# Kernel optimization log

Hardware: AMD Instinct MI355X
Metric: run time of the kernel (lower is better)

## Reference

```python
import jax, jax.numpy as jnp
import numpy as np
import math

B, S, D, H, HD, P = 2, 2048, 2048, 16, 128, 10
ROPE_BASE = 10000.0


def _rope_tables(seq_len, head_dim):
    inv_freq = 1.0 / (ROPE_BASE ** (np.arange(0, head_dim, 2, dtype=np.float32) / head_dim))
    t = np.arange(seq_len, dtype=np.float32)
    freqs = np.outer(t, inv_freq)                  # [S, hd/2]
    emb = np.concatenate([freqs, freqs], axis=-1)  # [S, hd]
    return jnp.asarray(np.cos(emb)), jnp.asarray(np.sin(emb))


def _rotate_half(x):
    half = x.shape[-1] // 2
    return jnp.concatenate([-x[..., half:], x[..., :half]], axis=-1)


def setup_inputs() -> dict:
    key = jax.random.key(0)
    ks = jax.random.split(key, 8)
    hidden_states = jax.random.normal(ks[0], (B, S, D), dtype=jnp.float32)
    # causal additive mask, llama convention: 0 where allowed, large negative above diagonal
    causal = jnp.triu(jnp.full((S, S), -1e9, dtype=jnp.float32), k=1)
    attention_mask = jnp.broadcast_to(causal[None, None], (B, 1, S, S))
    position_ids = jnp.broadcast_to(jnp.arange(S, dtype=jnp.int64)[None], (B, S))
    scale = 1.0 / math.sqrt(D)
    Wq = jax.random.normal(ks[1], (D, D), dtype=jnp.float32) * scale
    Wk = jax.random.normal(ks[2], (D, D), dtype=jnp.float32) * scale
    Wv = jax.random.normal(ks[3], (D, D), dtype=jnp.float32) * scale
    Wo = jax.random.normal(ks[4], (D, D), dtype=jnp.float32) * scale
    adapter_query = jax.random.normal(ks[5], (P, D), dtype=jnp.float32)
    adapter_gate = jax.random.normal(ks[6], (1, H, 1, 1), dtype=jnp.float32) * 0.1
    return dict(hidden_states=hidden_states, attention_mask=attention_mask,
                position_ids=position_ids, Wq=Wq, Wk=Wk, Wv=Wv, Wo=Wo,
                adapter_query=adapter_query, adapter_gate=adapter_gate)


def reference(hidden_states, attention_mask, position_ids, Wq, Wk, Wv, Wo,
              adapter_query, adapter_gate):
    bsz, q_len, _ = hidden_states.shape
    inv_sqrt_hd = 1.0 / math.sqrt(HD)

    def split_heads(x):  # [B,S,D] -> [B,H,S,hd]
        return x.reshape(bsz, q_len, H, HD).transpose(0, 2, 1, 3)

    q = split_heads(hidden_states @ Wq)
    k = split_heads(hidden_states @ Wk)
    v = split_heads(hidden_states @ Wv)

    # RoPE
    cos_t, sin_t = _rope_tables(q_len, HD)
    cos = cos_t[position_ids][:, None]  # [B,1,S,hd]
    sin = sin_t[position_ids][:, None]
    q = q * cos + _rotate_half(q) * sin
    k = k * cos + _rotate_half(k) * sin

    # main attention
    scores = jnp.einsum('bhqd,bhkd->bhqk', q, k) * inv_sqrt_hd
    scores = scores + attention_mask
    attn = jax.nn.softmax(scores.astype(jnp.float32), axis=-1).astype(q.dtype)
    attn_out = jnp.einsum('bhqk,bhkd->bhqd', attn, v)

    # adapter: soft prompt projected through k/v proj (learn_kv=False), no RoPE
    adapter = jnp.broadcast_to(adapter_query[None], (bsz, P, D))  # [B,P,D]
    a_k = (adapter @ Wk).reshape(bsz, P, H, HD).transpose(0, 2, 1, 3)  # [B,H,P,hd]
    a_v = (adapter @ Wv).reshape(bsz, P, H, HD).transpose(0, 2, 1, 3)
    a_scores = jnp.einsum('bhqd,bhpd->bhqp', q, a_k) * inv_sqrt_hd
    a_w = adapter_gate * jax.nn.softmax(a_scores.astype(jnp.float32), axis=-1).astype(q.dtype)
    a_out = jnp.einsum('bhqp,bhpd->bhqd', a_w, a_v)

    out = attn_out + a_out
    out = out.transpose(0, 2, 1, 3).reshape(bsz, q_len, D)
    return out @ Wo
```

## Files before the change

### kernel.cpp

```cpp
#include <hip/hip_runtime.h>
#include <cstdint>
#include <cstddef>
#include <cmath>

typedef __bf16 bf16x8 __attribute__((ext_vector_type(8)));
typedef float  f32x4  __attribute__((ext_vector_type(4)));

__device__ __forceinline__ unsigned short f2bf(float f) {
  unsigned int u = __float_as_uint(f);
  u += 0x7FFF + ((u >> 16) & 1);
  return (unsigned short)(u >> 16);
}
__device__ __forceinline__ float bf2f(unsigned short u) {
  return __uint_as_float(((unsigned int)u) << 16);
}

#define SEQ 2048
#define DMODEL 2048
#define NH 16
#define HD 128
#define NB 2
#define NP 10
#define MAUG 4106
#define SCALEL2 (0.08838834764831845f * 1.44269504088896340f)

#define GLOAD_LDS16(g, l) \
  __builtin_amdgcn_global_load_lds((__attribute__((address_space(1))) const void*)(g), \
                                   (__attribute__((address_space(3))) void*)(l), 16, 0, 0)

#define FENCE() asm volatile("" ::: "memory")
#define SBAR() do { FENCE(); __builtin_amdgcn_s_barrier(); FENCE(); } while (0)
#define WAITVM(N) asm volatile("s_waitcnt vmcnt(" #N ")" ::: "memory")

__global__ void k_tables(float* __restrict__ cost, float* __restrict__ sint) {
  int idx = blockIdx.x * 256 + threadIdx.x;
  if (idx >= SEQ * 64) return;
  int s = idx >> 6, i = idx & 63;
  float invf = expf(-((float)(2 * i) / 128.0f) * logf(10000.0f));
  float a = (float)s * invf;
  float c = cosf(a), sn = sinf(a);
  cost[s * HD + i] = c;  cost[s * HD + 64 + i] = c;
  sint[s * HD + i] = sn; sint[s * HD + 64 + i] = sn;
}

__global__ __launch_bounds__(256) void k_wt(const float* __restrict__ W0,
                                            const float* __restrict__ W1,
                                            const float* __restrict__ W2,
                                            const float* __restrict__ W3,
                                            unsigned short* __restrict__ out) {
  __shared__ float tile[64][65];
  const float* W = (blockIdx.z == 0) ? W0 : (blockIdx.z == 1) ? W1 : (blockIdx.z == 2) ? W2 : W3;
  unsigned short* o = out + (size_t)blockIdx.z * DMODEL * DMODEL;
  int bx = blockIdx.x * 64, by = blockIdx.y * 64;
  int c = threadIdx.x & 15, r0 = threadIdx.x >> 4;
  #pragma unroll
  for (int jj = 0; jj < 4; jj++) {
    int r = r0 + jj * 16;
    float4 v = *(const float4*)&W[(size_t)(bx + r) * DMODEL + by + c * 4];
    tile[r][c * 4 + 0] = v.x; tile[r][c * 4 + 1] = v.y;
    tile[r][c * 4 + 2] = v.z; tile[r][c * 4 + 3] = v.w;
  }
  __syncthreads();
  #pragma unroll
  for (int jj = 0; jj < 4; jj++) {
    int ro = r0 + jj * 16;
    unsigned short s4[4];
    #pragma unroll
    for (int k = 0; k < 4; k++) s4[k] = f2bf(tile[c * 4 + k][ro]);
    *(uint2*)&o[(size_t)(by + ro) * DMODEL + bx + c * 4] = *(const uint2*)s4;
  }
}

__global__ void k_xaug(const float* __restrict__ X, const float* __restrict__ Aq,
                       unsigned short* __restrict__ xaug) {
  size_t u = ((size_t)blockIdx.x * 256 + threadIdx.x) * 8;
  size_t row = u >> 11;
  int col = (int)(u & 2047);
  const float* src = (row < (size_t)NB * SEQ) ? &X[u]
                                              : &Aq[(row - NB * SEQ) * DMODEL + col];
  float4 a = *(const float4*)src;
  float4 b = *(const float4*)(src + 4);
  unsigned short r[8] = { f2bf(a.x), f2bf(a.y), f2bf(a.z), f2bf(a.w),
                          f2bf(b.x), f2bf(b.y), f2bf(b.z), f2bf(b.w) };
  *(uint4*)&xaug[u] = *(const uint4*)r;
}

#define RD_A(dst, bb, MH) do { \
  _Pragma("unroll") for (int i_ = 0; i_ < 4; i_++) \
    _Pragma("unroll") for (int ks_ = 0; ks_ < 2; ks_++) \
      dst[i_][ks_] = *(const bf16x8*)&lds[(bb) + (wr*128 + (MH)*64 + i_*16 + lr)*64 + (((ks_*4+quad) ^ (lr & 7)) * 8)]; \
} while (0)

#define RD_B(dst, bb, NHH) do { \
  _Pragma("unroll") for (int j_ = 0; j_ < 2; j_++) \
    _Pragma("unroll") for (int ks_ = 0; ks_ < 2; ks_++) \
      dst[j_][ks_] = *(const bf16x8*)&lds[(bb) + 16384 + (wc*64 + (NHH)*32 + j_*16 + lr)*64 + (((ks_*4+quad) ^ (lr & 7)) * 8)]; \
} while (0)

#define MM(A, B, MH, NHH) do { \
  __builtin_amdgcn_s_setprio(1); \
  _Pragma("unroll") for (int i_ = 0; i_ < 4; i_++) \
    _Pragma("unroll") for (int j_ = 0; j_ < 2; j_++) { \
      acc[(MH)*4+i_][(NHH)*2+j_] = __builtin_amdgcn_mfma_f32_16x16x32_bf16(A[i_][0], B[j_][0], acc[(MH)*4+i_][(NHH)*2+j_], 0, 0, 0); \
      acc[(MH)*4+i_][(NHH)*2+j_] = __builtin_amdgcn_mfma_f32_16x16x32_bf16(A[i_][1], B[j_][1], acc[(MH)*4+i_][(NHH)*2+j_], 0, 0, 0); \
    } \
  __builtin_amdgcn_s_setprio(0); \
} while (0)

#define STG_AE(nb, ko) do { \
  GLOAD_LDS16(sA + (ko),                      &lds[(nb)*32768 + (qrow)*64 + g8]); \
  GLOAD_LDS16(sA + 128*(size_t)DMODEL + (ko), &lds[(nb)*32768 + (128+qrow)*64 + g8]); } while (0)
#define STG_AO(nb, ko) do { \
  GLOAD_LDS16(sA + 64*(size_t)DMODEL + (ko),  &lds[(nb)*32768 + (64+qrow)*64 + g8]); \
  GLOAD_LDS16(sA + 192*(size_t)DMODEL + (ko), &lds[(nb)*32768 + (192+qrow)*64 + g8]); } while (0)
#define STG_BE(nb, ko) do { \
  GLOAD_LDS16(sB + (ko),                      &lds[(nb)*32768 + 16384 + (qb)*64 + g8]); \
  GLOAD_LDS16(sB + 128*(size_t)DMODEL + (ko), &lds[(nb)*32768 + 16384 + (128+qb)*64 + g8]); } while (0)
#define STG_BO(nb, ko) do { \
  GLOAD_LDS16(sB + 32*(size_t)DMODEL + (ko),  &lds[(nb)*32768 + 16384 + (32+qb)*64 + g8]); \
  GLOAD_LDS16(sB + 160*(size_t)DMODEL + (ko), &lds[(nb)*32768 + 16384 + (160+qb)*64 + g8]); } while (0)

template<int BF16OUT>
__global__ __launch_bounds__(512, 2) void k_gemm256(const unsigned short* __restrict__ A,
                                                    const unsigned short* __restrict__ Bt,
                                                    void* __restrict__ Cv,
                                                    int M, size_t c_stride_mat) {
  __shared__ unsigned short lds[65536];
  const int t = threadIdx.x;
  const int lane = t & 63, w = t >> 6;
  const int lr = lane & 15, quad = lane >> 4;
  const int wr = w >> 2, wc = w & 3;
  const int tm = (M + 255) >> 8;
  const int perz = tm * 8;
  const int qchunk = gridDim.x >> 3;
  const int lin = ((int)blockIdx.x & 7) * qchunk + ((int)blockIdx.x >> 3);
  const int z = lin / perz;
  const int rem = lin - z * perz;
  const int m0 = (rem >> 3) * 256, n0 = (rem & 7) * 256;
  const unsigned short* Bz = Bt + (size_t)z * DMODEL * DMODEL;

  const int qrow = t >> 3;
  const int g8 = (t & 7) * 8;
  const int gsw8 = (((t & 7) ^ (qrow & 7)) * 8);
  const int qb = (qrow < 32) ? qrow : qrow + 32;

  const unsigned short* sA = A + (size_t)(m0 + qrow) * DMODEL + gsw8;
  const unsigned short* sB = Bz + (size_t)(n0 + qb) * DMODEL + gsw8;

  bf16x8 aE[4][2], aO[4][2], bE[2][2], bO[2][2];
  f32x4 acc[8][4];
  #pragma unroll
  for (int i = 0; i < 8; i++)
    #pragma unroll
    for (int j = 0; j < 4; j++) acc[i][j] = (f32x4){0.f, 0.f, 0.f, 0.f};

  STG_AE(0, 0); STG_BE(0, 0); STG_BO(0, 0); STG_AO(0, 0);
  WAITVM(4);
  SBAR();
  RD_A(aE, 0, 0); RD_B(bE, 0, 0);

  for (int kt = 0; kt < DMODEL / 64; kt++) {
    const int base = (kt & 1) << 15;
    const int nb2 = (kt & 1) ^ 1;
    const int nbase = nb2 << 15;
    const int ko = (kt + 1) * 64;
    const bool more = (kt + 1 < DMODEL / 64);

    if (more) { STG_AE(nb2, ko); WAITVM(4); } else WAITVM(2);
    SBAR();
    RD_B(bO, base, 1);
    MM(aE, bE, 0, 0);

    if (more) { STG_BE(nb2, ko); WAITVM(4); } else WAITVM(0);
    SBAR();
    RD_A(aO, base, 1);
    MM(aE, bO, 0, 1);

    if (more) STG_BO(nb2, ko);
    MM(aO, bE, 1, 0);

    if (more) {
      STG_AO(nb2, ko);
      WAITVM(4);
      SBAR();
      RD_A(aE, nbase, 0); RD_B(bE, nbase, 0);
    }
    MM(aO, bO, 1, 1);
  }

  #pragma unroll
  for (int mi = 0; mi < 8; mi++) {
    #pragma unroll
    for (int r = 0; r < 4; r++) {
      int row = m0 + wr * 128 + mi * 16 + quad * 4 + r;
      if (row < M) {
        if (BF16OUT) {
          unsigned short* C = (unsigned short*)Cv + (size_t)z * c_stride_mat;
          #pragma unroll
          for (int n = 0; n < 4; n++)
            C[(size_t)row * DMODEL + n0 + wc * 64 + n * 16 + lr] = f2bf(acc[mi][n][r]);
        } else {
          float* C = (float*)Cv + (size_t)z * c_stride_mat;
          #pragma unroll
          for (int n = 0; n < 4; n++)
            C[(size_t)row * DMODEL + n0 + wc * 64 + n * 16 + lr] = acc[mi][n][r];
        }
      }
    }
  }
}

#define O_LDA(MH) do { \
  _Pragma("unroll") for (int i_ = 0; i_ < 2; i_++) \
    _Pragma("unroll") for (int ks_ = 0; ks_ < 2; ks_++) \
      a[i_][ks_] = *(const bf16x8*)&lds[base + (wr*64 + ((MH)*2+i_)*16 + lr)*64 + (((ks_*4+quad) ^ (lr & 7)) * 8)]; \
} while (0)

#define O_LDB(NHH) do { \
  _Pragma("unroll") for (int j_ = 0; j_ < 2; j_++) \
    _Pragma("unroll") for (int ks_ = 0; ks_ < 2; ks_++) \
      b[(NHH)*2+j_][ks_] = *(const bf16x8*)&lds[base + 8192 + (wc*64 + ((NHH)*2+j_)*16 + lr)*64 + (((ks_*4+quad) ^ (lr & 7)) * 8)]; \
} while (0)

#define O_MFMA(MH, NHH) do { \
  __builtin_amdgcn_s_setprio(1); \
  _Pragma("unroll") for (int i_ = 0; i_ < 2; i_++) \
    _Pragma("unroll") for (int j_ = 0; j_ < 2; j_++) { \
      acc[(MH)*2+i_][(NHH)*2+j_] = __builtin_amdgcn_mfma_f32_16x16x32_bf16(a[i_][0], b[(NHH)*2+j_][0], acc[(MH)*2+i_][(NHH)*2+j_], 0, 0, 0); \
      acc[(MH)*2+i_][(NHH)*2+j_] = __builtin_amdgcn_mfma_f32_16x16x32_bf16(a[i_][1], b[(NHH)*2+j_][1], acc[(MH)*2+i_][(NHH)*2+j_], 0, 0, 0); \
    } \
  __builtin_amdgcn_s_setprio(0); \
} while (0)

#define O_STG_AE(nb, ko) GLOAD_LDS16(sA + (ko), &lds[(nb)*24576 + (qb)*64 + g8])
#define O_STG_AO(nb, ko) GLOAD_LDS16(sA + 32*(size_t)DMODEL + (ko), &lds[(nb)*24576 + (32+qb)*64 + g8])
#define O_STG_BE(nb, ko) do { \
  GLOAD_LDS16(sB + (ko),                      &lds[(nb)*24576 + 8192 + (qb)*64 + g8]); \
  GLOAD_LDS16(sB + 128*(size_t)DMODEL + (ko), &lds[(nb)*24576 + 8192 + (128+qb)*64 + g8]); } while (0)
#define O_STG_BO(nb, ko) do { \
  GLOAD_LDS16(sB + 32*(size_t)DMODEL + (ko),  &lds[(nb)*24576 + 8192 + (32+qb)*64 + g8]); \
  GLOAD_LDS16(sB + 160*(size_t)DMODEL + (ko), &lds[(nb)*24576 + 8192 + (160+qb)*64 + g8]); } while (0)

__global__ __launch_bounds__(512, 2) void k_gemmo(const unsigned short* __restrict__ A,
                                                  const unsigned short* __restrict__ Bt,
                                                  float* __restrict__ C) {
  __shared__ unsigned short lds[49152];
  const int t = threadIdx.x;
  const int lane = t & 63, w = t >> 6;
  const int lr = lane & 15, quad = lane >> 4;
  const int wr = w >> 2, wc = w & 3;
  const int lin = ((int)blockIdx.x & 7) * 32 + ((int)blockIdx.x >> 3);
  const int m0 = (lin >> 3) * 128, n0 = (lin & 7) * 256;

  const int qrow = t >> 3;
  const int g8 = (t & 7) * 8;
  const int gsw8 = (((t & 7) ^ (qrow & 7)) * 8);
  const int qb = (qrow < 32) ? qrow : qrow + 32;

  const unsigned short* sA = A + (size_t)(m0 + qb) * DMODEL + gsw8;
  const unsigned short* sB = Bt + (size_t)(n0 + qb) * DMODEL + gsw8;

  bf16x8 a[2][2], b[4][2];
  f32x4 acc[4][4];
  #pragma unroll
  for (int i = 0; i < 4; i++)
    #pragma unroll
    for (int j = 0; j < 4; j++) acc[i][j] = (f32x4){0.f, 0.f, 0.f, 0.f};

  O_STG_AE(0, 0); O_STG_BE(0, 0); O_STG_BO(0, 0); O_STG_AO(0, 0);
  WAITVM(3);
  SBAR();

  for (int kt = 0; kt < DMODEL / 64; kt++) {
    const int base = (kt & 1) * 24576;
    const int nb = (kt & 1) ^ 1;
    const int ko = (kt + 1) * 64;
    const bool more = (kt + 1 < DMODEL / 64);

    O_LDA(0);
    O_LDB(0);
    if (more) O_STG_AE(nb, ko);
    SBAR();
    O_MFMA(0, 0);
    if (more) WAITVM(2); else WAITVM(1);
    SBAR();

    O_LDB(1);
    if (more) O_STG_BE(nb, ko);
    SBAR();
    O_MFMA(0, 1);
    if (more) WAITVM(3); else WAITVM(0);
    SBAR();

    O_LDA(1);
    if (more) O_STG_BO(nb, ko);
    SBAR();
    O_MFMA(1, 0);
    SBAR();

    if (more) O_STG_AO(nb, ko);
    SBAR();
    O_MFMA(1, 1);
    if (more) WAITVM(3);
    SBAR();
  }

  #pragma unroll
  for (int mi = 0; mi < 4; mi++) {
    #pragma unroll
    for (int r = 0; r < 4; r++) {
      int row = m0 + wr * 64 + mi * 16 + quad * 4 + r;
      #pragma unroll
      for (int n = 0; n < 4; n++)
        C[(size_t)row * DMODEL + n0 + wc * 64 + n * 16 + lr] = acc[mi][n][r];
    }
  }
}

__global__ __launch_bounds__(256) void k_ropevt(const unsigned short* __restrict__ Qf,
                                                const unsigned short* __restrict__ Kf,
                                                const unsigned short* __restrict__ Vf,
                                                const float* __restrict__ cost, const float* __restrict__ sint,
                                                unsigned short* __restrict__ Qb, unsigned short* __restrict__ Kb,
                                                unsigned short* __restrict__ AKb, unsigned short* __restrict__ avt,
                                                unsigned short* __restrict__ Vt) {
  __shared__ unsigned short tile[64][72];
  const int bid = blockIdx.x;
  const int t = threadIdx.x;
  if (bid < MAUG) {
    int row = bid;
    int c0 = t * 8;
    size_t off = (size_t)row * DMODEL + c0;
    if (row < NB * SEQ) {
      int s = row & (SEQ - 1);
      int d0 = c0 & (HD - 1);
      int po = (d0 < 64) ? 64 : -64;
      float sign = (d0 < 64) ? -1.f : 1.f;
      uint4 qv = *(const uint4*)&Qf[off];
      uint4 qp = *(const uint4*)&Qf[off + po];
      uint4 kv = *(const uint4*)&Kf[off];
      uint4 kp = *(const uint4*)&Kf[off + po];
      const unsigned short* qa = (const unsigned short*)&qv;
      const unsigned short* qb2 = (const unsigned short*)&qp;
      const unsigned short* ka = (const unsigned short*)&kv;
      const unsigned short* kb2 = (const unsigned short*)&kp;
      unsigned short oq[8], ok[8];
      #pragma unroll
      for (int j = 0; j < 8; j++) {
        float cv = cost[s * HD + d0 + j], sv = sint[s * HD + d0 + j];
        oq[j] = f2bf(bf2f(qa[j]) * cv + sign * bf2f(qb2[j]) * sv);
        ok[j] = f2bf(bf2f(ka[j]) * cv + sign * bf2f(kb2[j]) * sv);
      }
      *(uint4*)&Qb[off] = *(const uint4*)oq;
      *(uint4*)&Kb[off] = *(const uint4*)ok;
    } else {
      int p = row - NB * SEQ;
      uint4 kv = *(const uint4*)&Kf[off];
      uint4 vv = *(const uint4*)&Vf[off];
      *(uint4*)&AKb[(size_t)p * DMODEL + c0] = kv;
      const unsigned short* vp = (const unsigned short*)&vv;
      #pragma unroll
      for (int j = 0; j < 8; j++)
        avt[(size_t)(c0 + j) * 32 + p] = vp[j];
      if (p == 0) {
        #pragma unroll
        for (int j = 0; j < 8; j++)
          for (int pp = NP; pp < 32; pp++)
            avt[(size_t)(c0 + j) * 32 + pp] = 0;
      }
    }
  } else {
    int b2 = bid - MAUG;
    int s0 = (b2 & 31) * 64;
    int d0 = ((b2 >> 5) & 1) * 64;
    int z = b2 >> 6;
    int b = z >> 4, h = z & 15;
    #pragma unroll
    for (int j = t; j < 512; j += 256) {
      int row = j >> 3, ch = j & 7;
      *(uint4*)&tile[row][ch * 8] =
        *(const uint4*)&Vf[(size_t)(b * SEQ + s0 + row) * DMODEL + h * HD + d0 + ch * 8];
    }
    __syncthreads();
    #pragma unroll
    for (int j = t; j < 512; j += 256) {
      int dr = j >> 3, ch = j & 7;
      unsigned short tmp[8];
      #pragma unroll
      for (int k = 0; k < 8; k++) tmp[k] = tile[ch * 8 + k][dr];
      *(uint4*)&Vt[((size_t)((b * NH + h) * HD + d0 + dr)) * SEQ + s0 + ch * 8] = *(const uint4*)tmp;
    }
  }
}

#define PSTR 68

__global__ __launch_bounds__(256, 2) void k_flash(const unsigned short* __restrict__ Qb,
                                               const unsigned short* __restrict__ Kb,
                                               const unsigned short* __restrict__ Vt,
                                               const unsigned short* __restrict__ AKb,
                                               const unsigned short* __restrict__ avt,
                                               const float* __restrict__ gate,
                                               unsigned short* __restrict__ Obuf,
                                               float* __restrict__ ml,
                                               unsigned short* __restrict__ Aout) {
  const int L = blockIdx.x;
  const int h = L & 15;
  const int slot = 39 - (L >> 4);
  const int b = blockIdx.y;
  int qt, j, P;
  if (slot < 4)       { qt = slot;               j = 0;          P = 1; }
  else if (slot < 12) { int s = slot - 4;  qt = 4 + (s >> 1);  j = s & 1; P = 2; }
  else if (slot < 24) { int s = slot - 12; qt = 8 + s / 3;     j = s % 3; P = 3; }
  else                { int s = slot - 24; qt = 12 + (s >> 2); j = s & 3; P = 4; }

  const int t = threadIdx.x, w = t >> 6, lane = t & 63;
  const int lr = lane & 15, quad = lane >> 4;

  __shared__ unsigned short Ks[2 * 64 * 128];
  __shared__ unsigned short Vs[128 * 64];
  __shared__ unsigned short Ps[4][32 * PSTR];
  unsigned short* Ps16 = &Ps[w][0];

  const int row_base = qt * 128 + w * 32;

  bf16x8 qf[2][4];
  #pragma unroll
  for (int mt = 0; mt < 2; mt++)
    #pragma unroll
    for (int kk = 0; kk < 4; kk++)
      qf[mt][kk] = *(const bf16x8*)&Qb[((size_t)(b * SEQ + row_base + mt * 16 + lr)) * DMODEL
                                       + h * HD + kk * 32 + quad * 8];

  f32x4 o[2][8];
  #pragma unroll
  for (int mt = 0; mt < 2; mt++)
    #pragma unroll
    for (int nt = 0; nt < 8; nt++) o[mt][nt] = (f32x4){0.f, 0.f, 0.f, 0.f};
  float l_i[2][4];
  #pragma unroll
  for (int mt = 0; mt < 2; mt++)
    #pragma unroll
    for (int r = 0; r < 4; r++) l_i[mt][r] = 0.f;

  const int krow = t >> 4;
  const int vd = t >> 3, vc = (t & 7) ^ (vd & 7);
  const int ktend = 2 * qt + 2;

  #pragma unroll
  for (int jj = 0; jj < 4; jj++) {
    int row = krow + jj * 16;
    int c = (t & 15) ^ (row & 15);
    GLOAD_LDS16(&Kb[((size_t)(b * SEQ + j * 64 + row)) * DMODEL + h * HD + c * 8],
                &Ks[(t + jj * 256) * 8]);
  }
  #pragma unroll
  for (int jj = 0; jj < 4; jj++) {
    int d = vd + jj * 32;
    GLOAD_LDS16(&Vt[((size_t)((b * NH + h) * HD + d)) * SEQ + j * 64 + vc * 8],
                &Vs[(t + jj * 256) * 8]);
  }

  int kb = 0;
  for (int kt = j; kt < ktend; kt += P) {
    const bool more = (kt + P < ktend);
    const int kbase = kb * 8192;
    const int nkbase = 8192 - kbase;

    WAITVM(4);
    SBAR();

    f32x4 s4[2][4];
    #pragma unroll
// ... 131 lines not shown
        *(uint4*)&Aout[gb + rr * 128 + ch * 8] = *(const uint4*)&Ps16[rr * 128 + ch * 8];
      }
    }
  }

  #pragma unroll
  for (int mt = 0; mt < 2; mt++) {
    if (lr == 0) {
      #pragma unroll
      for (int r = 0; r < 4; r++) {
        int rl = w * 32 + mt * 16 + quad * 4 + r;
        ml[slotg * 128 + rl] = l_i[mt][r];
      }
    }
    #pragma unroll
    for (int nt = 0; nt < 8; nt++)
      #pragma unroll
      for (int r = 0; r < 4; r++)
        Ps16[(quad * 4 + r) * 128 + nt * 16 + lr] = f2bf(o[mt][nt][r]);
    size_t gb = slotg * 16384 + (size_t)(w * 32 + mt * 16) * 128;
    #pragma unroll
    for (int it = 0; it < 4; it++) {
      int i = lane + it * 64;
      int rr = i >> 4, ch = i & 15;
      *(uint4*)&Obuf[gb + rr * 128 + ch * 8] = *(const uint4*)&Ps16[rr * 128 + ch * 8];
    }
  }
}

__global__ __launch_bounds__(256) void k_merge(const unsigned short* __restrict__ Obuf,
                                               const float* __restrict__ ml,
                                               const unsigned short* __restrict__ Aout,
                                               unsigned short* __restrict__ ab) {
  int idx = blockIdx.x * 256 + threadIdx.x;
  int ch = idx & 15;
  int row = (idx >> 4) & 2047;
  int h = (idx >> 15) & 15;
  int b = idx >> 19;
  int qt = row >> 7, rl = row & 127;
  int start = qt < 4 ? qt : qt < 8 ? 4 + 2 * (qt - 4) : qt < 12 ? 12 + 3 * (qt - 8) : 24 + 4 * (qt - 12);
  int P = qt < 4 ? 1 : qt < 8 ? 2 : qt < 12 ? 3 : 4;
  size_t sbase = (size_t)(b * 16 + h) * 40 + start;
  float den = 0.f;
  float acc[8] = {0.f, 0.f, 0.f, 0.f, 0.f, 0.f, 0.f, 0.f};
  #pragma unroll
  for (int jp = 0; jp < 4; jp++) {
    if (jp < P) {
      den += ml[(sbase + jp) * 128 + rl];
      uint4 ov = *(const uint4*)&Obuf[(sbase + jp) * 16384 + rl * 128 + ch * 8];
      const unsigned short* pv = (const unsigned short*)&ov;
      #pragma unroll
      for (int k = 0; k < 8; k++) acc[k] += bf2f(pv[k]);
    }
  }
  uint4 av = *(const uint4*)&Aout[(((size_t)(b * 16 + h) * 16 + qt)) * 16384 + rl * 128 + ch * 8];
  const unsigned short* pa = (const unsigned short*)&av;
  float dn = 1.0f / den;
  unsigned short res[8];
  #pragma unroll
  for (int k = 0; k < 8; k++) res[k] = f2bf(acc[k] * dn + bf2f(pa[k]));
  *(uint4*)&ab[((size_t)(b * 2048 + row)) * 2048 + h * 128 + ch * 8] = *(const uint4*)res;
}

extern "C" void kernel_launch(void* const* d_in, const int* in_sizes, int n_in,
                              void* d_out, int out_size, void* d_ws, size_t ws_size,
                              hipStream_t stream) {
  const float* hidden = (const float*)d_in[0];
  const float* Wq = (const float*)d_in[3];
  const float* Wk = (const float*)d_in[4];
  const float* Wv = (const float*)d_in[5];
  const float* Wo = (const float*)d_in[6];
  const float* Aq = (const float*)d_in[7];
  const float* gate = (const float*)d_in[8];
  float* out = (float*)d_out;

  char* ws = (char*)d_ws;
  size_t off = 0;
  auto alloc = [&](size_t bytes) -> void* {
    void* p = ws + off;
    off = (off + bytes + 255) & ~(size_t)255;
    return p;
  };
  unsigned short* wt   = (unsigned short*)alloc((size_t)4 * DMODEL * DMODEL * 2);
  unsigned short* xaug = (unsigned short*)alloc((size_t)MAUG * DMODEL * 2);
  unsigned short* qkvb = (unsigned short*)alloc((size_t)3 * MAUG * DMODEL * 2);
  unsigned short* qf = qkvb;
  unsigned short* kf = qkvb + (size_t)MAUG * DMODEL;
  unsigned short* vf = kf + (size_t)MAUG * DMODEL;
  unsigned short* qb  = (unsigned short*)alloc((size_t)NB * SEQ * DMODEL * 2);
  unsigned short* kb  = (unsigned short*)alloc((size_t)NB * SEQ * DMODEL * 2);
  unsigned short* vt  = (unsigned short*)alloc((size_t)NB * SEQ * DMODEL * 2);
  unsigned short* akb = (unsigned short*)alloc((size_t)16 * DMODEL * 2);
  unsigned short* avt = (unsigned short*)alloc((size_t)DMODEL * 32 * 2);
  float* cost = (float*)alloc((size_t)SEQ * HD * 4);
  float* sint = (float*)alloc((size_t)SEQ * HD * 4);
  unsigned short* obuf = (unsigned short*)alloc((size_t)NB * NH * 40 * 16384 * 2);
  float* mlb = (float*)alloc((size_t)NB * NH * 40 * 128 * 4);
  unsigned short* aout = (unsigned short*)alloc((size_t)NB * NH * 16 * 16384 * 2);
  unsigned short* ab = qf;

  k_tables<<<SEQ * 64 / 256, 256, 0, stream>>>(cost, sint);
  k_wt<<<dim3(32, 32, 4), 256, 0, stream>>>(Wq, Wk, Wv, Wo, wt);
  k_xaug<<<4106, 256, 0, stream>>>(hidden, Aq, xaug);
  k_gemm256<1><<<dim3(408), 512, 0, stream>>>(xaug, wt, qkvb, MAUG, (size_t)MAUG * DMODEL);
  k_ropevt<<<MAUG + 2048, 256, 0, stream>>>(qf, kf, vf, cost, sint, qb, kb, akb, avt, vt);
  k_flash<<<dim3(640, 2), 256, 0, stream>>>(qb, kb, vt, akb, avt, gate, obuf, mlb, aout);
  k_merge<<<4096, 256, 0, stream>>>(obuf, mlb, aout, ab);
  k_gemmo<<<dim3(256), 512, 0, stream>>>(ab, wt + (size_t)3 * DMODEL * DMODEL, out);
}
```

Before: 403.1 us.

## Fuse prep kernels and restructure QKV GEMM into 4-stage K=32 pipeline

Merges the RoPE table, weight transpose/convert and input conversion kernels into one launch, removing two kernel launches and their tails. The 256x256 QKV GEMM drops its double-buffered K=64 ping-pong schedule for a 4-buffer ring of K=32 slices, prefetched three steps ahead, with a new XOR swizzle and one barrier per step. The intent is deeper load latency hiding and simpler scheduling. The cost is twice as many barriers per K and a different LDS bank-conflict pattern.

After: 410.7 us. Within noise of the previous version (+1.9%).

```diff
diff --git a/kernel.cpp b/kernel.cpp
--- a/kernel.cpp
+++ b/kernel.cpp
@@ -32,93 +32,78 @@
 #define SBAR() do { FENCE(); __builtin_amdgcn_s_barrier(); FENCE(); } while (0)
 #define WAITVM(N) asm volatile("s_waitcnt vmcnt(" #N ")" ::: "memory")
 
-__global__ void k_tables(float* __restrict__ cost, float* __restrict__ sint) {
-  int idx = blockIdx.x * 256 + threadIdx.x;
-  if (idx >= SEQ * 64) return;
-  int s = idx >> 6, i = idx & 63;
-  float invf = expf(-((float)(2 * i) / 128.0f) * logf(10000.0f));
-  float a = (float)s * invf;
-  float c = cosf(a), sn = sinf(a);
-  cost[s * HD + i] = c;  cost[s * HD + 64 + i] = c;
-  sint[s * HD + i] = sn; sint[s * HD + 64 + i] = sn;
-}
-
-__global__ __launch_bounds__(256) void k_wt(const float* __restrict__ W0,
-                                            const float* __restrict__ W1,
-                                            const float* __restrict__ W2,
-                                            const float* __restrict__ W3,
-                                            unsigned short* __restrict__ out) {
+__global__ __launch_bounds__(256) void k_prep(const float* __restrict__ W0,
+                                              const float* __restrict__ W1,
+                                              const float* __restrict__ W2,
+                                              const float* __restrict__ W3,
+                                              const float* __restrict__ X,
+                                              const float* __restrict__ Aq,
+                                              unsigned short* __restrict__ wt,
+                                              unsigned short* __restrict__ xaug,
+                                              float* __restrict__ cost,
+                                              float* __restrict__ sint) {
   __shared__ float tile[64][65];
-  const float* W = (blockIdx.z == 0) ? W0 : (blockIdx.z == 1) ? W1 : (blockIdx.z == 2) ? W2 : W3;
-  unsigned short* o = out + (size_t)blockIdx.z * DMODEL * DMODEL;
-  int bx = blockIdx.x * 64, by = blockIdx.y * 64;
-  int c = threadIdx.x & 15, r0 = threadIdx.x >> 4;
-  #pragma unroll
-  for (int jj = 0; jj < 4; jj++) {
-    int r = r0 + jj * 16;
-    float4 v = *(const float4*)&W[(size_t)(bx + r) * DMODEL + by + c * 4];
-    tile[r][c * 4 + 0] = v.x; tile[r][c * 4 + 1] = v.y;
-    tile[r][c * 4 + 2] = v.z; tile[r][c * 4 + 3] = v.w;
-  }
-  __syncthreads();
-  #pragma unroll
-  for (int jj = 0; jj < 4; jj++) {
-    int ro = r0 + jj * 16;
-    unsigned short s4[4];
-    #pragma unroll
-    for (int k = 0; k < 4; k++) s4[k] = f2bf(tile[c * 4 + k][ro]);
-    *(uint2*)&o[(size_t)(by + ro) * DMODEL + bx + c * 4] = *(const uint2*)s4;
-  }
-}
-
-__global__ void k_xaug(const float* __restrict__ X, const float* __restrict__ Aq,
-                       unsigned short* __restrict__ xaug) {
-  size_t u = ((size_t)blockIdx.x * 256 + threadIdx.x) * 8;
-  size_t row = u >> 11;
-  int col = (int)(u & 2047);
-  const float* src = (row < (size_t)NB * SEQ) ? &X[u]
-                                              : &Aq[(row - NB * SEQ) * DMODEL + col];
-  float4 a = *(const float4*)src;
-  float4 b = *(const float4*)(src + 4);
-  unsigned short r[8] = { f2bf(a.x), f2bf(a.y), f2bf(a.z), f2bf(a.w),
-                          f2bf(b.x), f2bf(b.y), f2bf(b.z), f2bf(b.w) };
-  *(uint4*)&xaug[u] = *(const uint4*)r;
-}
-
-#define RD_A(dst, bb, MH) do { \
-  _Pragma("unroll") for (int i_ = 0; i_ < 4; i_++) \
-    _Pragma("unroll") for (int ks_ = 0; ks_ < 2; ks_++) \
-      dst[i_][ks_] = *(const bf16x8*)&lds[(bb) + (wr*128 + (MH)*64 + i_*16 + lr)*64 + (((ks_*4+quad) ^ (lr & 7)) * 8)]; \
+  const int bid = blockIdx.x;
+  const int t = threadIdx.x;
+  if (bid < 512) {
+    int idx = bid * 256 + t;
+    int s = idx >> 6, i = idx & 63;
+    float invf = expf(-((float)(2 * i) / 128.0f) * logf(10000.0f));
+    float a = (float)s * invf;
+    float c = cosf(a), sn = sinf(a);
+    cost[s * HD + i] = c;  cost[s * HD + 64 + i] = c;
+    sint[s * HD + i] = sn; sint[s * HD + 64 + i] = sn;
+  } else if (bid < 512 + 4096) {
+    int wi = bid - 512;
+    int zw = wi >> 10, rem = wi & 1023;
+    const float* W = (zw == 0) ? W0 : (zw == 1) ? W1 : (zw == 2) ? W2 : W3;
+    unsigned short* o = wt + (size_t)zw * DMODEL * DMODEL;
+    int bx = (rem & 31) * 64, by = (rem >> 5) * 64;
+    int c = t & 15, r0 = t >> 4;
+    #pragma unroll
+    for (int jj = 0; jj < 4; jj++) {
+      int r = r0 + jj * 16;
+      float4 v = *(const float4*)&W[(size_t)(bx + r) * DMODEL + by + c * 4];
+      tile[r][c * 4 + 0] = v.x; tile[r][c * 4 + 1] = v.y;
+      tile[r][c * 4 + 2] = v.z; tile[r][c * 4 + 3] = v.w;
+    }
+    __syncthreads();
+    #pragma unroll
+    for (int jj = 0; jj < 4; jj++) {
+      int ro = r0 + jj * 16;
+      unsigned short s4[4];
+      #pragma unroll
+      for (int k = 0; k < 4; k++) s4[k] = f2bf(tile[c * 4 + k][ro]);
+      *(uint2*)&o[(size_t)(by + ro) * DMODEL + bx + c * 4] = *(const uint2*)s4;
+    }
+  } else {
+    int xi = bid - 4608;
+    size_t u = ((size_t)xi * 256 + t) * 8;
+    size_t row = u >> 11;
+    int col = (int)(u & 2047);
+    const float* src = (row < (size_t)NB * SEQ) ? &X[u]
+                                                : &Aq[(row - NB * SEQ) * DMODEL + col];
+    float4 a = *(const float4*)src;
+    float4 b = *(const float4*)(src + 4);
+    unsigned short r[8] = { f2bf(a.x), f2bf(a.y), f2bf(a.z), f2bf(a.w),
+                            f2bf(b.x), f2bf(b.y), f2bf(b.z), f2bf(b.w) };
+    *(uint4*)&xaug[u] = *(const uint4*)r;
+  }
+}
+
+#define G_RD() do { \
+  _Pragma("unroll") for (int mi_ = 0; mi_ < 8; mi_++) \
+    a[mi_] = *(const bf16x8*)&lds[bb + (wr*128 + mi_*16 + lr)*32 + rsw8]; \
+  _Pragma("unroll") for (int nj_ = 0; nj_ < 4; nj_++) \
+    b[nj_] = *(const bf16x8*)&lds[bb + 8192 + (wc*64 + nj_*16 + lr)*32 + rsw8]; \
 } while (0)
 
-#define RD_B(dst, bb, NHH) do { \
-  _Pragma("unroll") for (int j_ = 0; j_ < 2; j_++) \
-    _Pragma("unroll") for (int ks_ = 0; ks_ < 2; ks_++) \
-      dst[j_][ks_] = *(const bf16x8*)&lds[(bb) + 16384 + (wc*64 + (NHH)*32 + j_*16 + lr)*64 + (((ks_*4+quad) ^ (lr & 7)) * 8)]; \
+#define G_STG(bufi, ko) do { \
+  GLOAD_LDS16(sA + (ko),                      &lds[(bufi)*16384 + t*8]); \
+  GLOAD_LDS16(sA + 128*(size_t)DMODEL + (ko), &lds[(bufi)*16384 + 4096 + t*8]); \
+  GLOAD_LDS16(sB + (ko),                      &lds[(bufi)*16384 + 8192 + t*8]); \
+  GLOAD_LDS16(sB + 128*(size_t)DMODEL + (ko), &lds[(bufi)*16384 + 12288 + t*8]); \
 } while (0)
-
-#define MM(A, B, MH, NHH) do { \
-  __builtin_amdgcn_s_setprio(1); \
-  _Pragma("unroll") for (int i_ = 0; i_ < 4; i_++) \
-    _Pragma("unroll") for (int j_ = 0; j_ < 2; j_++) { \
-      acc[(MH)*4+i_][(NHH)*2+j_] = __builtin_amdgcn_mfma_f32_16x16x32_bf16(A[i_][0], B[j_][0], acc[(MH)*4+i_][(NHH)*2+j_], 0, 0, 0); \
-      acc[(MH)*4+i_][(NHH)*2+j_] = __builtin_amdgcn_mfma_f32_16x16x32_bf16(A[i_][1], B[j_][1], acc[(MH)*4+i_][(NHH)*2+j_], 0, 0, 0); \
-    } \
-  __builtin_amdgcn_s_setprio(0); \
-} while (0)
-
-#define STG_AE(nb, ko) do { \
-  GLOAD_LDS16(sA + (ko),                      &lds[(nb)*32768 + (qrow)*64 + g8]); \
-  GLOAD_LDS16(sA + 128*(size_t)DMODEL + (ko), &lds[(nb)*32768 + (128+qrow)*64 + g8]); } while (0)
-#define STG_AO(nb, ko) do { \
-  GLOAD_LDS16(sA + 64*(size_t)DMODEL + (ko),  &lds[(nb)*32768 + (64+qrow)*64 + g8]); \
-  GLOAD_LDS16(sA + 192*(size_t)DMODEL + (ko), &lds[(nb)*32768 + (192+qrow)*64 + g8]); } while (0)
-#define STG_BE(nb, ko) do { \
-  GLOAD_LDS16(sB + (ko),                      &lds[(nb)*32768 + 16384 + (qb)*64 + g8]); \
-  GLOAD_LDS16(sB + 128*(size_t)DMODEL + (ko), &lds[(nb)*32768 + 16384 + (128+qb)*64 + g8]); } while (0)
-#define STG_BO(nb, ko) do { \
-  GLOAD_LDS16(sB + 32*(size_t)DMODEL + (ko),  &lds[(nb)*32768 + 16384 + (32+qb)*64 + g8]); \
-  GLOAD_LDS16(sB + 160*(size_t)DMODEL + (ko), &lds[(nb)*32768 + 16384 + (160+qb)*64 + g8]); } while (0)
 
 template<int BF16OUT>
 __global__ __launch_bounds__(512, 2) void k_gemm256(const unsigned short* __restrict__ A,
@@ -130,6 +115,7 @@
   const int lane = t & 63, w = t >> 6;
   const int lr = lane & 15, quad = lane >> 4;
   const int wr = w >> 2, wc = w & 3;
+  const int rsw8 = (quad ^ ((lr >> 1) & 3)) * 8;
   const int tm = (M + 255) >> 8;
   const int perz = tm * 8;
   const int qchunk = gridDim.x >> 3;
@@ -139,53 +125,39 @@
   const int m0 = (rem >> 3) * 256, n0 = (rem & 7) * 256;
   const unsigned short* Bz = Bt + (size_t)z * DMODEL * DMODEL;
 
-  const int qrow = t >> 3;
-  const int g8 = (t & 7) * 8;
-  const int gsw8 = (((t & 7) ^ (qrow & 7)) * 8);
-  const int qb = (qrow < 32) ? qrow : qrow + 32;
-
-  const unsigned short* sA = A + (size_t)(m0 + qrow) * DMODEL + gsw8;
-  const unsigned short* sB = Bz + (size_t)(n0 + qb) * DMODEL + gsw8;
-
-  bf16x8 aE[4][2], aO[4][2], bE[2][2], bO[2][2];
+  const int srow = t >> 2;
+  const int scol8 = ((t & 3) ^ ((t >> 3) & 3)) * 8;
+  const unsigned short* sA = A + (size_t)(m0 + srow) * DMODEL + scol8;
+  const unsigned short* sB = Bz + (size_t)(n0 + srow) * DMODEL + scol8;
+
+  bf16x8 a[8], b[4];
   f32x4 acc[8][4];
   #pragma unroll
   for (int i = 0; i < 8; i++)
     #pragma unroll
     for (int j = 0; j < 4; j++) acc[i][j] = (f32x4){0.f, 0.f, 0.f, 0.f};
 
-  STG_AE(0, 0); STG_BE(0, 0); STG_BO(0, 0); STG_AO(0, 0);
-  WAITVM(4);
+  G_STG(0, 0); G_STG(1, 32); G_STG(2, 64);
+  WAITVM(8);
   SBAR();
-  RD_A(aE, 0, 0); RD_B(bE, 0, 0);
-
-  for (int kt = 0; kt < DMODEL / 64; kt++) {
-    const int base = (kt & 1) << 15;
-    const int nb2 = (kt & 1) ^ 1;
-    const int nbase = nb2 << 15;
-    const int ko = (kt + 1) * 64;
-    const bool more = (kt + 1 < DMODEL / 64);
-
-    if (more) { STG_AE(nb2, ko); WAITVM(4); } else WAITVM(2);
-    SBAR();
-    RD_B(bO, base, 1);
-    MM(aE, bE, 0, 0);
-
-    if (more) { STG_BE(nb2, ko); WAITVM(4); } else WAITVM(0);
-    SBAR();
-    RD_A(aO, base, 1);
-    MM(aE, bO, 0, 1);
-
-    if (more) STG_BO(nb2, ko);
-    MM(aO, bE, 1, 0);
-
-    if (more) {
-      STG_AO(nb2, ko);
-      WAITVM(4);
+
+  for (int kt = 0; kt < 64; kt++) {
+    const int bb = (kt & 3) * 16384;
+    G_RD();
+    if (kt < 61) G_STG((kt + 3) & 3, (kt + 3) * 32);
+    __builtin_amdgcn_s_setprio(1);
+    #pragma unroll
+    for (int mi = 0; mi < 8; mi++)
+      #pragma unroll
+      for (int nj = 0; nj < 4; nj++)
+        acc[mi][nj] = __builtin_amdgcn_mfma_f32_16x16x32_bf16(a[mi], b[nj], acc[mi][nj], 0, 0, 0);
+    __builtin_amdgcn_s_setprio(0);
+    if (kt < 63) {
+      if (kt < 61) WAITVM(8);
+      else if (kt == 61) WAITVM(4);
+      else WAITVM(0);
       SBAR();
-      RD_A(aE, nbase, 0); RD_B(bE, nbase, 0);
-    }
-    MM(aO, bO, 1, 1);
+    }
   }
 
   #pragma unroll
@@ -703,9 +675,7 @@
   unsigned short* aout = (unsigned short*)alloc((size_t)NB * NH * 16 * 16384 * 2);
   unsigned short* ab = qf;
 
-  k_tables<<<SEQ * 64 / 256, 256, 0, stream>>>(cost, sint);
-  k_wt<<<dim3(32, 32, 4), 256, 0, stream>>>(Wq, Wk, Wv, Wo, wt);
-  k_xaug<<<4106, 256, 0, stream>>>(hidden, Aq, xaug);
+  k_prep<<<512 + 4096 + 4106, 256, 0, stream>>>(Wq, Wk, Wv, Wo, hidden, Aq, wt, xaug, cost, sint);
   k_gemm256<1><<<dim3(408), 512, 0, stream>>>(xaug, wt, qkvb, MAUG, (size_t)MAUG * DMODEL);
   k_ropevt<<<MAUG + 2048, 256, 0, stream>>>(qf, kf, vf, cost, sint, qb, kb, akb, avt, vt);
   k_flash<<<dim3(640, 2), 256, 0, stream>>>(qb, kb, vt, akb, avt, gate, obuf, mlb, aout);
```

## Fuse RoPE and V transpose into QKV GEMM epilogue, merge prep kernels

Applied to the files above, without the earlier changes.

Three small preprocessing kernels (rope tables, weight transpose-to-bf16, input conversion) are merged into one launch. The separate RoPE/V-transpose pass is removed: the QKV GEMM epilogue now stages its tile in LDS, applies RoPE to Q/K, and writes V transposed and the adapter K/V directly. This avoids writing and rereading the intermediate QKV buffer and drops two launches. In exchange the GEMM epilogue gets extra LDS round trips, barriers and scattered cos/sin loads, and the xaug buffer is padded so the last row tile reads stay in bounds.

After: 398.9 us. No clear change (-1.0%).

```diff
diff --git a/kernel.cpp b/kernel.cpp
--- a/kernel.cpp
+++ b/kernel.cpp
@@ -32,57 +32,63 @@
 #define SBAR() do { FENCE(); __builtin_amdgcn_s_barrier(); FENCE(); } while (0)
 #define WAITVM(N) asm volatile("s_waitcnt vmcnt(" #N ")" ::: "memory")
 
-__global__ void k_tables(float* __restrict__ cost, float* __restrict__ sint) {
-  int idx = blockIdx.x * 256 + threadIdx.x;
-  if (idx >= SEQ * 64) return;
-  int s = idx >> 6, i = idx & 63;
-  float invf = expf(-((float)(2 * i) / 128.0f) * logf(10000.0f));
-  float a = (float)s * invf;
-  float c = cosf(a), sn = sinf(a);
-  cost[s * HD + i] = c;  cost[s * HD + 64 + i] = c;
-  sint[s * HD + i] = sn; sint[s * HD + 64 + i] = sn;
-}
-
-__global__ __launch_bounds__(256) void k_wt(const float* __restrict__ W0,
-                                            const float* __restrict__ W1,
-                                            const float* __restrict__ W2,
-                                            const float* __restrict__ W3,
-                                            unsigned short* __restrict__ out) {
+__global__ __launch_bounds__(256) void k_prep(const float* __restrict__ W0,
+                                              const float* __restrict__ W1,
+                                              const float* __restrict__ W2,
+                                              const float* __restrict__ W3,
+                                              const float* __restrict__ X,
+                                              const float* __restrict__ Aq,
+                                              unsigned short* __restrict__ wt,
+                                              unsigned short* __restrict__ xaug,
+                                              float* __restrict__ cost,
+                                              float* __restrict__ sint) {
   __shared__ float tile[64][65];
-  const float* W = (blockIdx.z == 0) ? W0 : (blockIdx.z == 1) ? W1 : (blockIdx.z == 2) ? W2 : W3;
-  unsigned short* o = out + (size_t)blockIdx.z * DMODEL * DMODEL;
-  int bx = blockIdx.x * 64, by = blockIdx.y * 64;
-  int c = threadIdx.x & 15, r0 = threadIdx.x >> 4;
-  #pragma unroll
-  for (int jj = 0; jj < 4; jj++) {
-    int r = r0 + jj * 16;
-    float4 v = *(const float4*)&W[(size_t)(bx + r) * DMODEL + by + c * 4];
-    tile[r][c * 4 + 0] = v.x; tile[r][c * 4 + 1] = v.y;
-    tile[r][c * 4 + 2] = v.z; tile[r][c * 4 + 3] = v.w;
-  }
-  __syncthreads();
-  #pragma unroll
-  for (int jj = 0; jj < 4; jj++) {
-    int ro = r0 + jj * 16;
-    unsigned short s4[4];
-    #pragma unroll
-    for (int k = 0; k < 4; k++) s4[k] = f2bf(tile[c * 4 + k][ro]);
-    *(uint2*)&o[(size_t)(by + ro) * DMODEL + bx + c * 4] = *(const uint2*)s4;
-  }
-}
-
-__global__ void k_xaug(const float* __restrict__ X, const float* __restrict__ Aq,
-                       unsigned short* __restrict__ xaug) {
-  size_t u = ((size_t)blockIdx.x * 256 + threadIdx.x) * 8;
-  size_t row = u >> 11;
-  int col = (int)(u & 2047);
-  const float* src = (row < (size_t)NB * SEQ) ? &X[u]
-                                              : &Aq[(row - NB * SEQ) * DMODEL + col];
-  float4 a = *(const float4*)src;
-  float4 b = *(const float4*)(src + 4);
-  unsigned short r[8] = { f2bf(a.x), f2bf(a.y), f2bf(a.z), f2bf(a.w),
-                          f2bf(b.x), f2bf(b.y), f2bf(b.z), f2bf(b.w) };
-  *(uint4*)&xaug[u] = *(const uint4*)r;
+  const int bid = blockIdx.x;
+  const int t = threadIdx.x;
+  if (bid < 512) {
+    int idx = bid * 256 + t;
+    int s = idx >> 6, i = idx & 63;
+    float invf = expf(-((float)(2 * i) / 128.0f) * logf(10000.0f));
+    float a = (float)s * invf;
+    float c = cosf(a), sn = sinf(a);
+    cost[s * HD + i] = c;  cost[s * HD + 64 + i] = c;
+    sint[s * HD + i] = sn; sint[s * HD + 64 + i] = sn;
+  } else if (bid < 512 + 4096) {
+    int wi = bid - 512;
+    int zw = wi >> 10, rem = wi & 1023;
+    const float* W = (zw == 0) ? W0 : (zw == 1) ? W1 : (zw == 2) ? W2 : W3;
+    unsigned short* o = wt + (size_t)zw * DMODEL * DMODEL;
+    int c = t & 15, r0 = t >> 4;
+    int bx = (rem & 31) * 64, by = (rem >> 5) * 64;
+    #pragma unroll
+    for (int jj = 0; jj < 4; jj++) {
+      int r = r0 + jj * 16;
+      float4 v = *(const float4*)&W[(size_t)(bx + r) * DMODEL + by + c * 4];
+      tile[r][c * 4 + 0] = v.x; tile[r][c * 4 + 1] = v.y;
+      tile[r][c * 4 + 2] = v.z; tile[r][c * 4 + 3] = v.w;
+    }
+    __syncthreads();
+    #pragma unroll
+    for (int jj = 0; jj < 4; jj++) {
+      int ro = r0 + jj * 16;
+      unsigned short s4[4];
+      #pragma unroll
+      for (int k = 0; k < 4; k++) s4[k] = f2bf(tile[c * 4 + k][ro]);
+      *(uint2*)&o[(size_t)(by + ro) * DMODEL + bx + c * 4] = *(const uint2*)s4;
+    }
+  } else {
+    int xi = bid - 4608;
+    size_t u = ((size_t)xi * 256 + t) * 8;
+    size_t row = u >> 11;
+    int col = (int)(u & 2047);
+    const float* src = (row < (size_t)NB * SEQ) ? &X[u]
+                                                : &Aq[(row - NB * SEQ) * DMODEL + col];
+    float4 a = *(const float4*)src;
+    float4 b = *(const float4*)(src + 4);
+    unsigned short r[8] = { f2bf(a.x), f2bf(a.y), f2bf(a.z), f2bf(a.w),
+                            f2bf(b.x), f2bf(b.y), f2bf(b.z), f2bf(b.w) };
+    *(uint4*)&xaug[u] = *(const uint4*)r;
+  }
 }
 
 #define RD_A(dst, bb, MH) do { \
@@ -114,23 +120,27 @@
   GLOAD_LDS16(sA + 64*(size_t)DMODEL + (ko),  &lds[(nb)*32768 + (64+qrow)*64 + g8]); \
   GLOAD_LDS16(sA + 192*(size_t)DMODEL + (ko), &lds[(nb)*32768 + (192+qrow)*64 + g8]); } while (0)
 #define STG_BE(nb, ko) do { \
-  GLOAD_LDS16(sB + (ko),                      &lds[(nb)*32768 + 16384 + (qb)*64 + g8]); \
-  GLOAD_LDS16(sB + 128*(size_t)DMODEL + (ko), &lds[(nb)*32768 + 16384 + (128+qb)*64 + g8]); } while (0)
+  GLOAD_LDS16(sB + (ko),                      &lds[(nb)*32768 + 16384 + (qbr)*64 + g8]); \
+  GLOAD_LDS16(sB + 128*(size_t)DMODEL + (ko), &lds[(nb)*32768 + 16384 + (128+qbr)*64 + g8]); } while (0)
 #define STG_BO(nb, ko) do { \
-  GLOAD_LDS16(sB + 32*(size_t)DMODEL + (ko),  &lds[(nb)*32768 + 16384 + (32+qb)*64 + g8]); \
-  GLOAD_LDS16(sB + 160*(size_t)DMODEL + (ko), &lds[(nb)*32768 + 16384 + (160+qb)*64 + g8]); } while (0)
-
-template<int BF16OUT>
-__global__ __launch_bounds__(512, 2) void k_gemm256(const unsigned short* __restrict__ A,
+  GLOAD_LDS16(sB + 32*(size_t)DMODEL + (ko),  &lds[(nb)*32768 + 16384 + (32+qbr)*64 + g8]); \
+  GLOAD_LDS16(sB + 160*(size_t)DMODEL + (ko), &lds[(nb)*32768 + 16384 + (160+qbr)*64 + g8]); } while (0)
+
+__global__ __launch_bounds__(512, 2) void k_gemmqkv(const unsigned short* __restrict__ A,
                                                     const unsigned short* __restrict__ Bt,
-                                                    void* __restrict__ Cv,
-                                                    int M, size_t c_stride_mat) {
+                                                    const float* __restrict__ cost,
+                                                    const float* __restrict__ sint,
+                                                    unsigned short* __restrict__ Qb,
+                                                    unsigned short* __restrict__ Kb,
+                                                    unsigned short* __restrict__ Vt,
+                                                    unsigned short* __restrict__ AKb,
+                                                    unsigned short* __restrict__ avt) {
   __shared__ unsigned short lds[65536];
   const int t = threadIdx.x;
   const int lane = t & 63, w = t >> 6;
   const int lr = lane & 15, quad = lane >> 4;
   const int wr = w >> 2, wc = w & 3;
-  const int tm = (M + 255) >> 8;
+  const int tm = (MAUG + 255) >> 8;
   const int perz = tm * 8;
   const int qchunk = gridDim.x >> 3;
   const int lin = ((int)blockIdx.x & 7) * qchunk + ((int)blockIdx.x >> 3);
@@ -142,10 +152,10 @@
   const int qrow = t >> 3;
   const int g8 = (t & 7) * 8;
   const int gsw8 = (((t & 7) ^ (qrow & 7)) * 8);
-  const int qb = (qrow < 32) ? qrow : qrow + 32;
+  const int qbr = (qrow < 32) ? qrow : qrow + 32;
 
   const unsigned short* sA = A + (size_t)(m0 + qrow) * DMODEL + gsw8;
-  const unsigned short* sB = Bz + (size_t)(n0 + qb) * DMODEL + gsw8;
+  const unsigned short* sB = Bz + (size_t)(n0 + qbr) * DMODEL + gsw8;
 
   bf16x8 aE[4][2], aO[4][2], bE[2][2], bO[2][2];
   f32x4 acc[8][4];
@@ -188,24 +198,101 @@
     MM(aO, bO, 1, 1);
   }
 
-  #pragma unroll
-  for (int mi = 0; mi < 8; mi++) {
-    #pragma unroll
-    for (int r = 0; r < 4; r++) {
-      int row = m0 + wr * 128 + mi * 16 + quad * 4 + r;
-      if (row < M) {
-        if (BF16OUT) {
-          unsigned short* C = (unsigned short*)Cv + (size_t)z * c_stride_mat;
+  const int rl0 = wr * 128;
+  const int cl0 = wc * 64;
+
+  if (z <= 1) {
+    if (m0 < NB * SEQ) {
+      unsigned short* dst = (z == 0) ? Qb : Kb;
+      SBAR();
+      #pragma unroll
+      for (int mi = 0; mi < 8; mi++)
+        #pragma unroll
+        for (int r = 0; r < 4; r++) {
+          int rl = rl0 + mi * 16 + quad * 4 + r;
+          int P = ((rl >> 2) & 7) << 3;
           #pragma unroll
-          for (int n = 0; n < 4; n++)
-            C[(size_t)row * DMODEL + n0 + wc * 64 + n * 16 + lr] = f2bf(acc[mi][n][r]);
-        } else {
-          float* C = (float*)Cv + (size_t)z * c_stride_mat;
+          for (int n = 0; n < 4; n++) {
+            int cl = cl0 + n * 16 + lr;
+            lds[rl * 256 + (cl ^ P)] = f2bf(acc[mi][n][r]);
+          }
+        }
+      SBAR();
+      #pragma unroll
+      for (int mi = 0; mi < 8; mi++)
+        #pragma unroll
+        for (int r = 0; r < 4; r++) {
+          int rl = rl0 + mi * 16 + quad * 4 + r;
+          int P = ((rl >> 2) & 7) << 3;
+          int srow = m0 + rl;
+          int s = srow & (SEQ - 1);
           #pragma unroll
-          for (int n = 0; n < 4; n++)
-            C[(size_t)row * DMODEL + n0 + wc * 64 + n * 16 + lr] = acc[mi][n][r];
+          for (int n = 0; n < 4; n++) {
+            int cl = cl0 + n * 16 + lr;
+            int d = cl & 127;
+            float v  = bf2f(lds[rl * 256 + (cl ^ P)]);
+            float vp = bf2f(lds[rl * 256 + ((cl ^ 64) ^ P)]);
+            float cv = cost[s * HD + d], sv = sint[s * HD + d];
+            float o = v * cv + ((d < 64) ? -vp : vp) * sv;
+            dst[(size_t)srow * DMODEL + n0 + cl] = f2bf(o);
+          }
         }
-      }
+    } else if (z == 1) {
+      #pragma unroll
+      for (int mi = 0; mi < 8; mi++)
+        #pragma unroll
+        for (int r = 0; r < 4; r++) {
+          int p = rl0 + mi * 16 + quad * 4 + r;
+          if (p < NP) {
+            #pragma unroll
+            for (int n = 0; n < 4; n++)
+              AKb[(size_t)p * DMODEL + n0 + cl0 + n * 16 + lr] = f2bf(acc[mi][n][r]);
+          }
+        }
+    }
+  } else {
+    if (m0 < NB * SEQ) {
+      SBAR();
+      #pragma unroll
+      for (int mi = 0; mi < 8; mi++)
+        #pragma unroll
+        for (int r = 0; r < 4; r++) {
+          int rl = rl0 + mi * 16 + quad * 4 + r;
+          #pragma unroll
+          for (int n = 0; n < 4; n++) {
+            int cl = cl0 + n * 16 + lr;
+            lds[cl * 256 + (rl ^ ((cl & 7) << 3))] = f2bf(acc[mi][n][r]);
+          }
+        }
+      SBAR();
+      const int bidx = m0 >> 11;
+      const int scol = m0 & 2047;
+      #pragma unroll
+      for (int rep = 0; rep < 4; rep++) {
+        int dr = (t >> 3) + rep * 64;
+        int hh = (n0 + dr) >> 7, dd = (n0 + dr) & 127;
+        size_t vbase = ((size_t)((bidx * NH + hh) * HD + dd)) * SEQ + scol;
+        #pragma unroll
+        for (int i = 0; i < 4; i++) {
+          int s0 = (t & 7) * 8 + i * 64;
+          int lbase = dr * 256 + (s0 ^ ((dr & 7) << 3));
+          *(uint4*)&Vt[vbase + s0] = *(const uint4*)&lds[lbase];
+        }
+      }
+    } else {
+      #pragma unroll
+      for (int mi = 0; mi < 8; mi++)
+        #pragma unroll
+        for (int r = 0; r < 4; r++) {
+          int p = rl0 + mi * 16 + quad * 4 + r;
+          if (p < 32) {
+            #pragma unroll
+            for (int n = 0; n < 4; n++) {
+              int cl = cl0 + n * 16 + lr;
+              avt[(size_t)(n0 + cl) * 32 + p] = (p < NP) ? f2bf(acc[mi][n][r]) : (unsigned short)0;
+            }
+          }
+        }
     }
   }
 }
@@ -313,82 +400,6 @@
       #pragma unroll
       for (int n = 0; n < 4; n++)
         C[(size_t)row * DMODEL + n0 + wc * 64 + n * 16 + lr] = acc[mi][n][r];
-    }
-  }
-}
-
-__global__ __launch_bounds__(256) void k_ropevt(const unsigned short* __restrict__ Qf,
-                                                const unsigned short* __restrict__ Kf,
-                                                const unsigned short* __restrict__ Vf,
-                                                const float* __restrict__ cost, const float* __restrict__ sint,
-                                                unsigned short* __restrict__ Qb, unsigned short* __restrict__ Kb,
-                                                unsigned short* __restrict__ AKb, unsigned short* __restrict__ avt,
-                                                unsigned short* __restrict__ Vt) {
-  __shared__ unsigned short tile[64][72];
-  const int bid = blockIdx.x;
-  const int t = threadIdx.x;
-  if (bid < MAUG) {
-    int row = bid;
-    int c0 = t * 8;
-    size_t off = (size_t)row * DMODEL + c0;
-    if (row < NB * SEQ) {
-      int s = row & (SEQ - 1);
-      int d0 = c0 & (HD - 1);
-      int po = (d0 < 64) ? 64 : -64;
-      float sign = (d0 < 64) ? -1.f : 1.f;
-      uint4 qv = *(const uint4*)&Qf[off];
-      uint4 qp = *(const uint4*)&Qf[off + po];
-      uint4 kv = *(const uint4*)&Kf[off];
-      uint4 kp = *(const uint4*)&Kf[off + po];
-      const unsigned short* qa = (const unsigned short*)&qv;
-      const unsigned short* qb2 = (const unsigned short*)&qp;
-      const unsigned short* ka = (const unsigned short*)&kv;
-      const unsigned short* kb2 = (const unsigned short*)&kp;
-      unsigned short oq[8], ok[8];
-      #pragma unroll
-      for (int j = 0; j < 8; j++) {
-        float cv = cost[s * HD + d0 + j], sv = sint[s * HD + d0 + j];
-        oq[j] = f2bf(bf2f(qa[j]) * cv + sign * bf2f(qb2[j]) * sv);
-        ok[j] = f2bf(bf2f(ka[j]) * cv + sign * bf2f(kb2[j]) * sv);
-      }
-      *(uint4*)&Qb[off] = *(const uint4*)oq;
-      *(uint4*)&Kb[off] = *(const uint4*)ok;
-    } else {
-      int p = row - NB * SEQ;
-      uint4 kv = *(const uint4*)&Kf[off];
-      uint4 vv = *(const uint4*)&Vf[off];
-      *(uint4*)&AKb[(size_t)p * DMODEL + c0] = kv;
-      const unsigned short* vp = (const unsigned short*)&vv;
-      #pragma unroll
-      for (int j = 0; j < 8; j++)
-        avt[(size_t)(c0 + j) * 32 + p] = vp[j];
-      if (p == 0) {
-        #pragma unroll
-        for (int j = 0; j < 8; j++)
-          for (int pp = NP; pp < 32; pp++)
-            avt[(size_t)(c0 + j) * 32 + pp] = 0;
-      }
-    }
-  } else {
-    int b2 = bid - MAUG;
-    int s0 = (b2 & 31) * 64;
-    int d0 = ((b2 >> 5) & 1) * 64;
-    int z = b2 >> 6;
-    int b = z >> 4, h = z & 15;
-    #pragma unroll
-    for (int j = t; j < 512; j += 256) {
-      int row = j >> 3, ch = j & 7;
-      *(uint4*)&tile[row][ch * 8] =
-        *(const uint4*)&Vf[(size_t)(b * SEQ + s0 + row) * DMODEL + h * HD + d0 + ch * 8];
-    }
-    __syncthreads();
-    #pragma unroll
-    for (int j = t; j < 512; j += 256) {
-      int dr = j >> 3, ch = j & 7;
-      unsigned short tmp[8];
-      #pragma unroll
-      for (int k = 0; k < 8; k++) tmp[k] = tile[ch * 8 + k][dr];
-      *(uint4*)&Vt[((size_t)((b * NH + h) * HD + d0 + dr)) * SEQ + s0 + ch * 8] = *(const uint4*)tmp;
     }
   }
 }
@@ -686,11 +697,7 @@
     return p;
   };
   unsigned short* wt   = (unsigned short*)alloc((size_t)4 * DMODEL * DMODEL * 2);
-  unsigned short* xaug = (unsigned short*)alloc((size_t)MAUG * DMODEL * 2);
-  unsigned short* qkvb = (unsigned short*)alloc((size_t)3 * MAUG * DMODEL * 2);
-  unsigned short* qf = qkvb;
-  unsigned short* kf = qkvb + (size_t)MAUG * DMODEL;
-  unsigned short* vf = kf + (size_t)MAUG * DMODEL;
+  unsigned short* xaug = (unsigned short*)alloc((size_t)(MAUG + 256) * DMODEL * 2);
   unsigned short* qb  = (unsigned short*)alloc((size_t)NB * SEQ * DMODEL * 2);
   unsigned short* kb  = (unsigned short*)alloc((size_t)NB * SEQ * DMODEL * 2);
   unsigned short* vt  = (unsigned short*)alloc((size_t)NB * SEQ * DMODEL * 2);
@@ -701,13 +708,10 @@
   unsigned short* obuf = (unsigned short*)alloc((size_t)NB * NH * 40 * 16384 * 2);
   float* mlb = (float*)alloc((size_t)NB * NH * 40 * 128 * 4);
   unsigned short* aout = (unsigned short*)alloc((size_t)NB * NH * 16 * 16384 * 2);
-  unsigned short* ab = qf;
-
-  k_tables<<<SEQ * 64 / 256, 256, 0, stream>>>(cost, sint);
-  k_wt<<<dim3(32, 32, 4), 256, 0, stream>>>(Wq, Wk, Wv, Wo, wt);
-  k_xaug<<<4106, 256, 0, stream>>>(hidden, Aq, xaug);
-  k_gemm256<1><<<dim3(408), 512, 0, stream>>>(xaug, wt, qkvb, MAUG, (size_t)MAUG * DMODEL);
-  k_ropevt<<<MAUG + 2048, 256, 0, stream>>>(qf, kf, vf, cost, sint, qb, kb, akb, avt, vt);
+  unsigned short* ab = xaug;
+
+  k_prep<<<512 + 4096 + 4106, 256, 0, stream>>>(Wq, Wk, Wv, Wo, hidden, Aq, wt, xaug, cost, sint);
+  k_gemmqkv<<<dim3(408), 512, 0, stream>>>(xaug, wt, cost, sint, qb, kb, vt, akb, avt);
   k_flash<<<dim3(640, 2), 256, 0, stream>>>(qb, kb, vt, akb, avt, gate, obuf, mlb, aout);
   k_merge<<<4096, 256, 0, stream>>>(obuf, mlb, aout, ab);
   k_gemmo<<<dim3(256), 512, 0, stream>>>(ab, wt + (size_t)3 * DMODEL * DMODEL, out);
```
